# Performance work log

Measured on AMD Instinct MI355X. Metric: run time of the kernel, lower is better.

The kernel has to match this reference:

```python
import jax, jax.numpy as jnp
import numpy as np

B, T, E, H, V = 32, 128, 512, 1024, 32000


def setup_inputs() -> dict:
    key = jax.random.key(0)
    ks = jax.random.split(key, 14)
    s = 0.02  # param init scale to keep gates in a sane range
    return {
        "features": jax.random.normal(ks[0], (B, E), jnp.float32),
        "captions": jax.random.randint(ks[1], (B, T), 0, V, jnp.int64),
        "embed_table": jax.random.normal(ks[2], (V, E), jnp.float32) * s,
        "pos_enc": jax.random.normal(ks[3], (1, T, E), jnp.float32) * s,
        "W_ih0": jax.random.normal(ks[4], (4 * H, E), jnp.float32) * s,
        "W_hh0": jax.random.normal(ks[5], (4 * H, H), jnp.float32) * s,
        "b_ih0": jax.random.normal(ks[6], (4 * H,), jnp.float32) * s,
        "b_hh0": jax.random.normal(ks[7], (4 * H,), jnp.float32) * s,
        "W_ih1": jax.random.normal(ks[8], (4 * H, H), jnp.float32) * s,
        "W_hh1": jax.random.normal(ks[9], (4 * H, H), jnp.float32) * s,
        "b_ih1": jax.random.normal(ks[10], (4 * H,), jnp.float32) * s,
        "b_hh1": jax.random.normal(ks[11], (4 * H,), jnp.float32) * s,
        "W_out": jax.random.normal(ks[12], (V, H), jnp.float32) * s,
        "b_out": jax.random.normal(ks[13], (V,), jnp.float32) * s,
    }


def _lstm_cell(h, c, x, W_ih, W_hh, b_ih, b_hh):
    # PyTorch gate order: i, f, g, o
    g = x @ W_ih.T + b_ih + h @ W_hh.T + b_hh  # (B, 4H)
    i, f, gg, o = jnp.split(g, 4, axis=-1)
    c_new = jax.nn.sigmoid(f) * c + jax.nn.sigmoid(i) * jnp.tanh(gg)
    h_new = jax.nn.sigmoid(o) * jnp.tanh(c_new)
    return h_new, c_new


def reference(features, captions, embed_table, pos_enc,
              W_ih0, W_hh0, b_ih0, b_hh0,
              W_ih1, W_hh1, b_ih1, b_hh1,
              W_out, b_out):
    # Teacher forcing ratio = 1.0 (the default): the input at step t is
    # captions[:, t-1], so the whole sequence of inputs is known upfront.
    bsz, seqlen = captions.shape
    hdim = W_hh0.shape[1]
    vocab = W_out.shape[0]
    dt = embed_table.dtype

    # Embedding lookup for all steps; only pos_enc[:, :1, :] is ever added.
    x = embed_table[captions[:, : seqlen - 1]] + pos_enc[0, 0]  # (B, T-1, E)
    x = jnp.swapaxes(x, 0, 1)  # (T-1, B, E) time-major for scan

    h0 = jnp.zeros((bsz, hdim), dt)
    c0 = jnp.zeros((bsz, hdim), dt)
    h1 = jnp.zeros((bsz, hdim), dt)
    c1 = jnp.zeros((bsz, hdim), dt)

    def step(carry, x_t):
        h0, c0, h1, c1 = carry
        h0, c0 = _lstm_cell(h0, c0, x_t, W_ih0, W_hh0, b_ih0, b_hh0)
        h1, c1 = _lstm_cell(h1, c1, h0, W_ih1, W_hh1, b_ih1, b_hh1)
        return (h0, c0, h1, c1), h1

    _, hs = jax.lax.scan(step, (h0, c0, h1, c1), x)  # (T-1, B, H)

    # One big GEMM for the decode projection of all steps.
    logits = jnp.einsum('tbh,vh->btv', hs, W_out) + b_out  # (B, T-1, V)
    outputs = jnp.concatenate(
        [jnp.zeros((bsz, 1, vocab), dt), logits], axis=1)  # outputs[:,0,:]=0
    return outputs
```

## Files before the change

kernel.cpp:

```cpp
#include <hip/hip_runtime.h>
#include <hip/hip_bf16.h>
#include <math.h>

typedef __attribute__((ext_vector_type(4))) float f32x4;
typedef __attribute__((ext_vector_type(8))) short s16x8;
typedef __attribute__((ext_vector_type(4))) unsigned short u16x4;

#define MFMA16(a, b, c) __builtin_amdgcn_mfma_f32_16x16x32_bf16(a, b, c, 0, 0, 0)

static constexpr int BB = 32, TT = 128, EE = 512, HH = 1024, VV = 32000;
static constexpr int FH = 4 * HH;
static constexpr int MROWS = (TT - 1) * BB;
static constexpr int MPAD = 4096;
static constexpr int BH = BB * HH;
static constexpr int NBLK = 256;

__device__ __forceinline__ unsigned short f2bf(float f) {
  unsigned int u = __float_as_uint(f);
  u = (u + 0x7FFFu + ((u >> 16) & 1u)) >> 16;
  return (unsigned short)u;
}
__device__ __forceinline__ float sigf(float x) { return 1.f / (1.f + __expf(-x)); }

__device__ __forceinline__ s16x8 pack8f(const float* p) {
  float4 x = *(const float4*)p;
  float4 y = *(const float4*)(p + 4);
  s16x8 r;
  r[0] = (short)f2bf(x.x); r[1] = (short)f2bf(x.y);
  r[2] = (short)f2bf(x.z); r[3] = (short)f2bf(x.w);
  r[4] = (short)f2bf(y.x); r[5] = (short)f2bf(y.y);
  r[6] = (short)f2bf(y.z); r[7] = (short)f2bf(y.w);
  return r;
}

__device__ __forceinline__ void gl_lds16(const void* g, void* l) {
  __builtin_amdgcn_global_load_lds(
      (const __attribute__((address_space(1))) unsigned int*)g,
      (__attribute__((address_space(3))) unsigned int*)l, 16, 0, 0);
}

__device__ __forceinline__ unsigned ldflag(const unsigned int* p) {
  return __hip_atomic_load(p, __ATOMIC_RELAXED, __HIP_MEMORY_SCOPE_AGENT);
}


__global__ void zero2_k(uint4* __restrict__ p0, int n0, uint4* __restrict__ p1, int n1) {
  int i = blockIdx.x * blockDim.x + threadIdx.x;
  int stride = gridDim.x * blockDim.x;
  uint4 z = {0u, 0u, 0u, 0u};
  for (int k = i; k < n0; k += stride) p0[k] = z;
  for (int k = i; k < n1; k += stride) p1[k] = z;
}

__global__ void cvt2_k(const float4* __restrict__ a, u16x4* __restrict__ ao, int na4,
                       const float4* __restrict__ b, u16x4* __restrict__ bo, int nb4) {
  int i = blockIdx.x * blockDim.x + threadIdx.x;
  int stride = gridDim.x * blockDim.x;
  for (int k = i; k < na4; k += stride) {
    float4 v = a[k];
    u16x4 o;
    o[0] = f2bf(v.x); o[1] = f2bf(v.y); o[2] = f2bf(v.z); o[3] = f2bf(v.w);
    ao[k] = o;
  }
  for (int k = i; k < nb4; k += stride) {
    float4 v = b[k];
    u16x4 o;
    o[0] = f2bf(v.x); o[1] = f2bf(v.y); o[2] = f2bf(v.z); o[3] = f2bf(v.w);
    bo[k] = o;
  }
}

__global__ __launch_bounds__(256) void embed_k(const int* __restrict__ captions,
                                               const float* __restrict__ etab,
                                               const float* __restrict__ pos,
                                               unsigned short* __restrict__ X) {
  const int m = blockIdx.x;
  const int t = m >> 5, b = m & 31;
  if (t < TT - 1) {
    const int tok = captions[b * TT + t];
    const float* er = etab + (size_t)tok * EE;
    for (int e = threadIdx.x; e < EE; e += 256)
      X[(size_t)m * EE + e] = f2bf(er[e] + pos[e]);
  } else {
    for (int e = threadIdx.x; e < EE; e += 256) X[(size_t)m * EE + e] = 0;
  }
}

__global__ void zero_out_t0(float* __restrict__ out) {
  out[(size_t)blockIdx.y * TT * VV + blockIdx.x * 256 + threadIdx.x] = 0.f;
}


__global__ __launch_bounds__(256) void gemm_bt(const unsigned short* __restrict__ A,
                                               const unsigned short* __restrict__ Bm,
                                               int K, int N,
                                               const float* __restrict__ bias0,
                                               const float* __restrict__ bias1,
                                               float* __restrict__ Cout) {
  __shared__ unsigned short As[128 * 64];
  __shared__ unsigned short Bs[128 * 64];
  const int tid = threadIdx.x;
  const int lane = tid & 63, wave = tid >> 6;
  const int wm = wave & 1, wn = wave >> 1;
  const int m0 = blockIdx.x * 128, n0 = blockIdx.y * 128;
  const int sch = (lane & 7) * 8;
  const int srbase = wave * 32 + (lane >> 3);
  f32x4 acc[4][4] = {};

  for (int k0 = 0; k0 < K; k0 += 64) {
    __syncthreads();
#pragma unroll
    for (int i = 0; i < 4; ++i) {
      const int r = srbase + i * 8;
      gl_lds16(&A[(size_t)(m0 + r) * K + k0 + sch], &As[(wave * 4 + i) * 512]);
      gl_lds16(&Bm[(size_t)(n0 + r) * K + k0 + sch], &Bs[(wave * 4 + i) * 512]);
    }
    __syncthreads();
#pragma unroll
    for (int kk = 0; kk < 64; kk += 32) {
      s16x8 af[4], bf[4];
#pragma unroll
      for (int f = 0; f < 4; ++f) {
        af[f] = *(const s16x8*)(&As[(wm * 64 + f * 16 + (lane & 15)) * 64 + kk + (lane >> 4) * 8]);
        bf[f] = *(const s16x8*)(&Bs[(wn * 64 + f * 16 + (lane & 15)) * 64 + kk + (lane >> 4) * 8]);
      }
#pragma unroll
      for (int mi = 0; mi < 4; ++mi)
#pragma unroll
        for (int ni = 0; ni < 4; ++ni)
          acc[mi][ni] = MFMA16(af[mi], bf[ni], acc[mi][ni]);
    }
  }

#pragma unroll
  for (int mi = 0; mi < 4; ++mi) {
#pragma unroll
    for (int ni = 0; ni < 4; ++ni) {
      const int col = n0 + wn * 64 + ni * 16 + (lane & 15);
      float bs = bias0[col] + bias1[col];
      const int mbase = m0 + wm * 64 + mi * 16 + (lane >> 4) * 4;
#pragma unroll
      for (int r = 0; r < 4; ++r) {
        int m = mbase + r;
        if (m < MROWS) Cout[(size_t)m * N + col] = acc[mi][ni][r] + bs;
      }
    }
  }
}


__global__ __launch_bounds__(512, 1) void proj_gemm(const unsigned short* __restrict__ hsA,
                                                    const unsigned short* __restrict__ Woutb,
                                                    const float* __restrict__ bout,
                                                    float* __restrict__ out) {
  __shared__ unsigned short As[256 * 64];
  __shared__ unsigned short Bs[256 * 64];
  const int tid = threadIdx.x;
  const int lane = tid & 63, wave = tid >> 6;
  const int wm = wave & 1, wn = wave >> 1;
  const int T = blockIdx.x;
  const int j = T / 125, n = T % 125;
  const int m0 = j * 256, n0 = n * 256;
  const int sch = (lane & 7) * 8;
  const int rbase = tid >> 3;
  f32x4 acc[8][4] = {};

  for (int k0 = 0; k0 < HH; k0 += 64) {
    __syncthreads();
#pragma unroll
    for (int i = 0; i < 4; ++i) {
      const int r = rbase + i * 64;
      gl_lds16(&hsA[(size_t)(m0 + r) * HH + k0 + sch], &As[(wave * 64 + i * 512) * 8]);
      gl_lds16(&Woutb[(size_t)(n0 + r) * HH + k0 + sch], &Bs[(wave * 64 + i * 512) * 8]);
    }
    __syncthreads();
#pragma unroll
    for (int kk = 0; kk < 64; kk += 32) {
      s16x8 af[8], bf[4];
#pragma unroll
      for (int f = 0; f < 8; ++f)
        af[f] = *(const s16x8*)(&As[(wm * 128 + f * 16 + (lane & 15)) * 64 + kk + (lane >> 4) * 8]);
#pragma unroll
      for (int f = 0; f < 4; ++f)
        bf[f] = *(const s16x8*)(&Bs[(wn * 64 + f * 16 + (lane & 15)) * 64 + kk + (lane >> 4) * 8]);
#pragma unroll
      for (int mi = 0; mi < 8; ++mi)
#pragma unroll
        for (int ni = 0; ni < 4; ++ni)
          acc[mi][ni] = MFMA16(af[mi], bf[ni], acc[mi][ni]);
    }
  }

#pragma unroll
  for (int mi = 0; mi < 8; ++mi) {
#pragma unroll
    for (int ni = 0; ni < 4; ++ni) {
      const int col = n0 + wn * 64 + ni * 16 + (lane & 15);
      const float bs = bout[col];
      const int mbase = m0 + wm * 128 + mi * 16 + (lane >> 4) * 4;
#pragma unroll
      for (int r2 = 0; r2 < 4; ++r2) {
        const int m = mbase + r2;
        if (m < MROWS) {
          const int tt = m >> 5, b2 = m & 31;
          out[((size_t)b2 * TT + tt + 1) * VV + col] = acc[mi][ni][r2] + bs;
        }
      }
    }
  }
}


__global__ __launch_bounds__(256, 1) void lstm_persist(
    const float* __restrict__ Whh0f, const float* __restrict__ Wih1f,
    const float* __restrict__ Whh1f, const float* __restrict__ G0pre,
    const float* __restrict__ bih1, const float* __restrict__ bhh1,
    unsigned short* __restrict__ h0seq, unsigned short* __restrict__ hseq1,
    unsigned short* __restrict__ hs_all,
    unsigned int* __restrict__ flags0, unsigned int* __restrict__ flags1) {
  __shared__ float parts[4][2][2][16][16];
  const int bid = blockIdx.x;
  const int layer = bid >> 7;
  const int blk = bid & 127;
  const int tid = threadIdx.x, lane = tid & 63, wave = tid >> 6;
  const int jb = blk * 8;
  const int colIdx = lane & 15;
  const int kq = lane >> 4;
  const int wrow0 = (colIdx >> 3) * HH + jb + (colIdx & 7);

  const int cb = tid >> 3, cjj = tid & 7;
  float creg = 0.f;
  float bsum[4];
  if (layer == 1) {
#pragma unroll
    for (int gi = 0; gi < 4; ++gi)
      bsum[gi] = bih1[gi * HH + jb + cjj] + bhh1[gi * HH + jb + cjj];
  }

  s16x8 wreg[16][2];
  const int kb = (layer == 0) ? wave * 256 : (wave & 1) * 512;
  if (layer == 0) {
#pragma unroll
    for (int fi = 0; fi < 2; ++fi) {
      const float* wp = Whh0f + (size_t)(wrow0 + fi * 2 * HH) * HH + kb + kq * 8;
#pragma unroll
      for (int ks = 0; ks < 8; ++ks) wreg[ks][fi] = pack8f(wp + ks * 32);
    }
  } else {
    const float* Wsrc = (wave < 2) ? Wih1f : Whh1f;
#pragma unroll
    for (int fi = 0; fi < 2; ++fi) {
      const float* wp = Wsrc + (size_t)(wrow0 + fi * 2 * HH) * HH + kb + kq * 8;
#pragma unroll
      for (int ks = 0; ks < 16; ++ks) wreg[ks][fi] = pack8f(wp + ks * 32);
    }
  }

  const int frag_off = (kb >> 3) * 256 + kq * 256 + (lane & 15) * 8;

  if (layer == 0) {
    for (int t = 0; t < TT - 1; ++t) {
      float gpre[4];
#pragma unroll
      for (int gi = 0; gi < 4; ++gi)
        gpre[gi] = G0pre[((size_t)t * BB + cb) * FH + gi * HH + jb + cjj];

      if (t > 0 && wave == 0) {
        const unsigned tgt = (unsigned)t;
        for (;;) {
          unsigned a = ldflag(&flags0[(lane * 2 + 0) * 32]);
          unsigned b = ldflag(&flags0[(lane * 2 + 1) * 32]);
          if (__all(min(a, b) >= tgt)) break;
          __builtin_amdgcn_s_sleep(1);
        }
      }
      __syncthreads();
      asm volatile("" ::: "memory");

      const unsigned short* a0 = h0seq + (size_t)t * BH + frag_off;
      const unsigned short* a1 = a0 + 128;
      f32x4 acc00 = {}, acc01 = {}, acc10 = {}, acc11 = {};
#pragma unroll
      for (int ks = 0; ks < 8; ++ks) {
        s16x8 av0 = *(const s16x8*)(a0 + ks * 1024);
        s16x8 av1 = *(const s16x8*)(a1 + ks * 1024);
        acc00 = MFMA16(av0, wreg[ks][0], acc00);
        acc01 = MFMA16(av0, wreg[ks][1], acc01);
        acc10 = MFMA16(av1, wreg[ks][0], acc10);
        acc11 = MFMA16(av1, wreg[ks][1], acc11);
      }
#pragma unroll
      for (int r = 0; r < 4; ++r) {
        parts[wave][0][0][kq * 4 + r][colIdx] = acc00[r];
        parts[wave][0][1][kq * 4 + r][colIdx] = acc01[r];
        parts[wave][1][0][kq * 4 + r][colIdx] = acc10[r];
        parts[wave][1][1][kq * 4 + r][colIdx] = acc11[r];
      }
      __syncthreads();
      float g[4];
#pragma unroll
      for (int gi = 0; gi < 4; ++gi) {
        float s = gpre[gi];
        const int fi = gi >> 1, c = (gi & 1) * 8 + cjj;
#pragma unroll
        for (int w4 = 0; w4 < 4; ++w4) s += parts[w4][cb >> 4][fi][cb & 15][c];
        g[gi] = s;
      }
      const float i_ = sigf(g[0]), f_ = sigf(g[1]), gg = tanhf(g[2]), o_ = sigf(g[3]);
      creg = f_ * creg + i_ * gg;
      *(volatile unsigned short*)&h0seq[(size_t)(t + 1) * BH + blk * 256 + tid] =
          f2bf(o_ * tanhf(creg));

      asm volatile("s_waitcnt vmcnt(0)" ::: "memory");
      __syncthreads();
      if (tid == 0) *(volatile unsigned int*)&flags0[blk * 32] = (unsigned)(t + 1);
    }
  } else {
    for (int t = 1; t < TT; ++t) {
      if (wave == 0) {
        const unsigned t0 = (unsigned)t, t1 = (unsigned)(t - 1);
        for (;;) {
          unsigned a0 = ldflag(&flags0[(lane * 2 + 0) * 32]);
          unsigned b0 = ldflag(&flags0[(lane * 2 + 1) * 32]);
          unsigned a1 = ldflag(&flags1[(lane * 2 + 0) * 32]);
          unsigned b1 = ldflag(&flags1[(lane * 2 + 1) * 32]);
          bool ok = (min(a0, b0) >= t0) && (min(a1, b1) >= t1);
          if (__all(ok)) break;
          __builtin_amdgcn_s_sleep(1);
        }
      }
      __syncthreads();
      asm volatile("" ::: "memory");

      const unsigned short* base = (wave < 2)
                                       ? (h0seq + (size_t)t * BH)
                                       : (hseq1 + (size_t)(t - 1) * BH);
      const unsigned short* a0 = base + frag_off;
      const unsigned short* a1 = a0 + 128;
      f32x4 acc00 = {}, acc01 = {}, acc10 = {}, acc11 = {};
#pragma unroll
      for (int ks = 0; ks < 16; ++ks) {
        s16x8 av0 = *(const s16x8*)(a0 + ks * 1024);
        s16x8 av1 = *(const s16x8*)(a1 + ks * 1024);
        acc00 = MFMA16(av0, wreg[ks][0], acc00);
        acc01 = MFMA16(av0, wreg[ks][1], acc01);
        acc10 = MFMA16(av1, wreg[ks][0], acc10);
        acc11 = MFMA16(av1, wreg[ks][1], acc11);
      }
#pragma unroll
      for (int r = 0; r < 4; ++r) {
        parts[wave][0][0][kq * 4 + r][colIdx] = acc00[r];
        parts[wave][0][1][kq * 4 + r][colIdx] = acc01[r];
        parts[wave][1][0][kq * 4 + r][colIdx] = acc10[r];
        parts[wave][1][1][kq * 4 + r][colIdx] = acc11[r];
      }
      __syncthreads();
      float g[4];
#pragma unroll
      for (int gi = 0; gi < 4; ++gi) {
        float s = bsum[gi];
        const int fi = gi >> 1, c = (gi & 1) * 8 + cjj;
#pragma unroll
        for (int w4 = 0; w4 < 4; ++w4) s += parts[w4][cb >> 4][fi][cb & 15][c];
        g[gi] = s;
      }
      const float i_ = sigf(g[0]), f_ = sigf(g[1]), gg = tanhf(g[2]), o_ = sigf(g[3]);
      creg = f_ * creg + i_ * gg;
      const unsigned short hv = f2bf(o_ * tanhf(creg));
      *(volatile unsigned short*)&hseq1[(size_t)t * BH + blk * 256 + tid] = hv;
      hs_all[(size_t)t * BH + (size_t)cb * HH + jb + cjj] = hv;

      asm volatile("s_waitcnt vmcnt(0)" ::: "memory");
      __syncthreads();
      if (tid == 0) *(volatile unsigned int*)&flags1[blk * 32] = (unsigned)t;
    }
  }
}


extern "C" void kernel_launch(void* const* d_in, const int* in_sizes, int n_in,
                              void* d_out, int out_size, void* d_ws, size_t ws_size,
                              hipStream_t stream) {
  const int* captions = (const int*)d_in[1];
  const float* etab = (const float*)d_in[2];
  const float* pos = (const float*)d_in[3];
  const float* Wih0 = (const float*)d_in[4];
  const float* Whh0 = (const float*)d_in[5];
  const float* bih0 = (const float*)d_in[6];
  const float* bhh0 = (const float*)d_in[7];
  const float* Wih1 = (const float*)d_in[8];
  const float* Whh1 = (const float*)d_in[9];
  const float* bih1 = (const float*)d_in[10];
  const float* bhh1 = (const float*)d_in[11];
  const float* Wout = (const float*)d_in[12];
  const float* bout = (const float*)d_in[13];
  float* out = (float*)d_out;

  char* w = (char*)d_ws;
  auto alloc = [&](size_t bytes) {
    char* p = w;
    w += (bytes + 255) & ~(size_t)255;
    return p;
  };
  unsigned int* flags0 = (unsigned int*)alloc(128 * 128);
  unsigned int* flags1 = (unsigned int*)alloc(128 * 128);
  unsigned short* h0seq = (unsigned short*)alloc((size_t)TT * BH * 2);
  unsigned short* hseq1 = (unsigned short*)alloc((size_t)TT * BH * 2);
  unsigned short* hs_all = (unsigned short*)alloc((size_t)4160 * HH * 2);

  unsigned short* Xb = (unsigned short*)alloc((size_t)MPAD * EE * 2);
  unsigned short* Wih0b = (unsigned short*)alloc((size_t)FH * EE * 2);
  unsigned short* Woutb = (unsigned short*)alloc((size_t)VV * HH * 2);
  float* G0pre = (float*)alloc((size_t)MROWS * FH * 4);

  hipLaunchKernelGGL(zero2_k, dim3(40), dim3(256), 0, stream,
                     (uint4*)flags0, (int)((128 * 128 * 2 + BH * 2) / 16),
                     (uint4*)hseq1, (int)((BH * 2) / 16));
  hipLaunchKernelGGL(cvt2_k, dim3(4096), dim3(256), 0, stream,
                     (const float4*)Wih0, (u16x4*)Wih0b, FH * EE / 4,
                     (const float4*)Wout, (u16x4*)Woutb, VV * HH / 4);
  hipLaunchKernelGGL(embed_k, dim3(MPAD), dim3(256), 0, stream, captions, etab, pos, Xb);
  hipLaunchKernelGGL(gemm_bt, dim3(32, 32), dim3(256), 0, stream, Xb, Wih0b, EE, FH, bih0,
                     bhh0, G0pre);
  hipLaunchKernelGGL(lstm_persist, dim3(NBLK), dim3(256), 0, stream, Whh0, Wih1, Whh1, G0pre,
                     bih1, bhh1, h0seq, hseq1, hs_all, flags0, flags1);
  hipLaunchKernelGGL(proj_gemm, dim3(16 * 125), dim3(512), 0, stream, hs_all + (size_t)BH,
                     Woutb, bout, out);
  hipLaunchKernelGGL(zero_out_t0, dim3(125, 32), dim3(256), 0, stream, out);
}
```

Baseline: 1.354 ms.

## Double-buffer projection GEMM LDS and make recurrent waves poll flags independently

The output projection GEMM now keeps two LDS buffers and prefetches the next K tile while issuing MFMAs on the current one, so global-to-LDS loads overlap compute. In the persistent LSTM recurrence, every wave now spins on the flags it needs itself instead of wave 0 polling and then a block-wide barrier. In layer 1, the waves reading h0 wait only on layer-0 flags and the waves reading h1 wait only on layer-1 flags, which decouples their progress. This doubles LDS use in the GEMM and adds more polling traffic per block in the recurrence.

```diff
diff --git a/kernel.cpp b/kernel.cpp
--- a/kernel.cpp
+++ b/kernel.cpp
@@ -153,8 +153,8 @@
                                                     const unsigned short* __restrict__ Woutb,
                                                     const float* __restrict__ bout,
                                                     float* __restrict__ out) {
-  __shared__ unsigned short As[256 * 64];
-  __shared__ unsigned short Bs[256 * 64];
+  __shared__ unsigned short As[2][256 * 64];
+  __shared__ unsigned short Bs[2][256 * 64];
   const int tid = threadIdx.x;
   const int lane = tid & 63, wave = tid >> 6;
   const int wm = wave & 1, wn = wave >> 1;
@@ -165,29 +165,41 @@
   const int rbase = tid >> 3;
   f32x4 acc[8][4] = {};
 
-  for (int k0 = 0; k0 < HH; k0 += 64) {
-    __syncthreads();
+  auto stageP = [&](int k0, int buf) {
 #pragma unroll
     for (int i = 0; i < 4; ++i) {
       const int r = rbase + i * 64;
-      gl_lds16(&hsA[(size_t)(m0 + r) * HH + k0 + sch], &As[(wave * 64 + i * 512) * 8]);
-      gl_lds16(&Woutb[(size_t)(n0 + r) * HH + k0 + sch], &Bs[(wave * 64 + i * 512) * 8]);
-    }
-    __syncthreads();
+      gl_lds16(&hsA[(size_t)(m0 + r) * HH + k0 + sch], &As[buf][(wave * 64 + i * 512) * 8]);
+      gl_lds16(&Woutb[(size_t)(n0 + r) * HH + k0 + sch], &Bs[buf][(wave * 64 + i * 512) * 8]);
+    }
+  };
+
+  stageP(0, 0);
+  asm volatile("s_waitcnt vmcnt(0)" ::: "memory");
+  __syncthreads();
+  int cur = 0;
+
+  for (int ks = 0; ks < 16; ++ks) {
+    if (ks < 15) stageP((ks + 1) * 64, cur ^ 1);
 #pragma unroll
     for (int kk = 0; kk < 64; kk += 32) {
       s16x8 af[8], bf[4];
 #pragma unroll
       for (int f = 0; f < 8; ++f)
-        af[f] = *(const s16x8*)(&As[(wm * 128 + f * 16 + (lane & 15)) * 64 + kk + (lane >> 4) * 8]);
+        af[f] = *(const s16x8*)(&As[cur][(wm * 128 + f * 16 + (lane & 15)) * 64 + kk + (lane >> 4) * 8]);
 #pragma unroll
       for (int f = 0; f < 4; ++f)
-        bf[f] = *(const s16x8*)(&Bs[(wn * 64 + f * 16 + (lane & 15)) * 64 + kk + (lane >> 4) * 8]);
+        bf[f] = *(const s16x8*)(&Bs[cur][(wn * 64 + f * 16 + (lane & 15)) * 64 + kk + (lane >> 4) * 8]);
 #pragma unroll
       for (int mi = 0; mi < 8; ++mi)
 #pragma unroll
         for (int ni = 0; ni < 4; ++ni)
           acc[mi][ni] = MFMA16(af[mi], bf[ni], acc[mi][ni]);
+    }
+    if (ks < 15) {
+      asm volatile("s_waitcnt vmcnt(0)" ::: "memory");
+      __syncthreads();
+      cur ^= 1;
     }
   }
 
@@ -265,7 +277,7 @@
       for (int gi = 0; gi < 4; ++gi)
         gpre[gi] = G0pre[((size_t)t * BB + cb) * FH + gi * HH + jb + cjj];
 
-      if (t > 0 && wave == 0) {
+      if (t > 0) {
         const unsigned tgt = (unsigned)t;
         for (;;) {
           unsigned a = ldflag(&flags0[(lane * 2 + 0) * 32]);
@@ -274,7 +286,6 @@
           __builtin_amdgcn_s_sleep(1);
         }
       }
-      __syncthreads();
       asm volatile("" ::: "memory");
 
       const unsigned short* a0 = h0seq + (size_t)t * BH + frag_off;
@@ -317,19 +328,23 @@
     }
   } else {
     for (int t = 1; t < TT; ++t) {
-      if (wave == 0) {
-        const unsigned t0 = (unsigned)t, t1 = (unsigned)(t - 1);
+      if (wave < 2) {
+        const unsigned t0 = (unsigned)t;
         for (;;) {
-          unsigned a0 = ldflag(&flags0[(lane * 2 + 0) * 32]);
-          unsigned b0 = ldflag(&flags0[(lane * 2 + 1) * 32]);
-          unsigned a1 = ldflag(&flags1[(lane * 2 + 0) * 32]);
-          unsigned b1 = ldflag(&flags1[(lane * 2 + 1) * 32]);
-          bool ok = (min(a0, b0) >= t0) && (min(a1, b1) >= t1);
-          if (__all(ok)) break;
+          unsigned a = ldflag(&flags0[(lane * 2 + 0) * 32]);
+          unsigned b = ldflag(&flags0[(lane * 2 + 1) * 32]);
+          if (__all(min(a, b) >= t0)) break;
           __builtin_amdgcn_s_sleep(1);
         }
-      }
-      __syncthreads();
+      } else {
+        const unsigned t1 = (unsigned)(t - 1);
+        for (;;) {
+          unsigned a = ldflag(&flags1[(lane * 2 + 0) * 32]);
+          unsigned b = ldflag(&flags1[(lane * 2 + 1) * 32]);
+          if (__all(min(a, b) >= t1)) break;
+          __builtin_amdgcn_s_sleep(1);
+        }
+      }
       asm volatile("" ::: "memory");
 
       const unsigned short* base = (wave < 2)
```

Measured after the change: 1.390 ms. +2.6%, slower.

## Double-buffer LDS in output projection GEMM and remap block tiles for reuse

Applied to the files above, without the earlier changes.

The projection GEMM now uses two LDS buffers and prefetches the next K-slice with global-to-LDS loads while MFMAs run on the current one. This overlaps memory latency with compute and removes one barrier per iteration. It also remaps block indices so consecutive blocks share the same W_out column tile across M tiles, which should improve L2 reuse of the large weight matrix. LDS use doubles to 128KB per block, which still fits at one block per CU.

```diff
diff --git a/kernel.cpp b/kernel.cpp
--- a/kernel.cpp
+++ b/kernel.cpp
@@ -153,41 +153,55 @@
                                                     const unsigned short* __restrict__ Woutb,
                                                     const float* __restrict__ bout,
                                                     float* __restrict__ out) {
-  __shared__ unsigned short As[256 * 64];
-  __shared__ unsigned short Bs[256 * 64];
+  __shared__ unsigned short As[2][256 * 64];
+  __shared__ unsigned short Bs[2][256 * 64];
   const int tid = threadIdx.x;
   const int lane = tid & 63, wave = tid >> 6;
   const int wm = wave & 1, wn = wave >> 1;
   const int T = blockIdx.x;
-  const int j = T / 125, n = T % 125;
+  const int bq = T & 15;
+  const int j = 2 * (bq & 7) + (bq >> 3);
+  const int n = T >> 4;
   const int m0 = j * 256, n0 = n * 256;
   const int sch = (lane & 7) * 8;
   const int rbase = tid >> 3;
   f32x4 acc[8][4] = {};
 
-  for (int k0 = 0; k0 < HH; k0 += 64) {
-    __syncthreads();
+  auto stageP = [&](int k0, int buf) {
 #pragma unroll
     for (int i = 0; i < 4; ++i) {
       const int r = rbase + i * 64;
-      gl_lds16(&hsA[(size_t)(m0 + r) * HH + k0 + sch], &As[(wave * 64 + i * 512) * 8]);
-      gl_lds16(&Woutb[(size_t)(n0 + r) * HH + k0 + sch], &Bs[(wave * 64 + i * 512) * 8]);
-    }
-    __syncthreads();
+      gl_lds16(&hsA[(size_t)(m0 + r) * HH + k0 + sch], &As[buf][(wave * 64 + i * 512) * 8]);
+      gl_lds16(&Woutb[(size_t)(n0 + r) * HH + k0 + sch], &Bs[buf][(wave * 64 + i * 512) * 8]);
+    }
+  };
+
+  stageP(0, 0);
+  asm volatile("s_waitcnt vmcnt(0)" ::: "memory");
+  __syncthreads();
+  int cur = 0;
+
+  for (int ks = 0; ks < 16; ++ks) {
+    if (ks < 15) stageP((ks + 1) * 64, cur ^ 1);
 #pragma unroll
     for (int kk = 0; kk < 64; kk += 32) {
       s16x8 af[8], bf[4];
 #pragma unroll
       for (int f = 0; f < 8; ++f)
-        af[f] = *(const s16x8*)(&As[(wm * 128 + f * 16 + (lane & 15)) * 64 + kk + (lane >> 4) * 8]);
+        af[f] = *(const s16x8*)(&As[cur][(wm * 128 + f * 16 + (lane & 15)) * 64 + kk + (lane >> 4) * 8]);
 #pragma unroll
       for (int f = 0; f < 4; ++f)
-        bf[f] = *(const s16x8*)(&Bs[(wn * 64 + f * 16 + (lane & 15)) * 64 + kk + (lane >> 4) * 8]);
+        bf[f] = *(const s16x8*)(&Bs[cur][(wn * 64 + f * 16 + (lane & 15)) * 64 + kk + (lane >> 4) * 8]);
 #pragma unroll
       for (int mi = 0; mi < 8; ++mi)
 #pragma unroll
         for (int ni = 0; ni < 4; ++ni)
           acc[mi][ni] = MFMA16(af[mi], bf[ni], acc[mi][ni]);
+    }
+    if (ks < 15) {
+      asm volatile("s_waitcnt vmcnt(0)" ::: "memory");
+      __syncthreads();
+      cur ^= 1;
     }
   }
 
@@ -424,7 +438,7 @@
                      bhh0, G0pre);
   hipLaunchKernelGGL(lstm_persist, dim3(NBLK), dim3(256), 0, stream, Whh0, Wih1, Whh1, G0pre,
                      bih1, bhh1, h0seq, hseq1, hs_all, flags0, flags1);
-  hipLaunchKernelGGL(proj_gemm, dim3(16 * 125), dim3(512), 0, stream, hs_all + (size_t)BH,
+  hipLaunchKernelGGL(proj_gemm, dim3(2000), dim3(512), 0, stream, hs_all + (size_t)BH,
                      Woutb, bout, out);
   hipLaunchKernelGGL(zero_out_t0, dim3(125, 32), dim3(256), 0, stream, out);
 }
```

Result: no change. 1.356 ms (+0.1%).
